# Kernel optimization log

Measured on AMD Instinct MI355X. Metric: run time of the kernel, lower is better.

Reference implementation:

```python
import jax, jax.numpy as jnp
import numpy as np

HID = 64
HEADS = 4
HEAD_DIM = HID // HEADS
N_MOL, N_PROT = 2048, 4096
E_MOL, E_PROT = 32768, 131072
B = 32


def _lin(key, din, dout):
    kw, kb = jax.random.split(key)
    s = 1.0 / np.sqrt(din)
    W = jax.random.uniform(kw, (din, dout), jnp.float32, -s, s)
    b = jax.random.uniform(kb, (dout,), jnp.float32, -s, s)
    return W, b


def setup_inputs() -> dict:
    key = jax.random.key(0)
    ks = jax.random.split(key, 32)
    inp = {}
    inp['mol_x'] = jax.random.normal(ks[0], (N_MOL, 11), jnp.float32)
    inp['prot_x'] = jax.random.normal(ks[1], (N_PROT, 15), jnp.float32)
    inp['mol_eattr'] = jax.random.normal(ks[2], (E_MOL, 10), jnp.float32)
    inp['prot_eattr'] = jax.random.normal(ks[3], (E_PROT, 10), jnp.float32)
    inp['mol_edge_index'] = jax.random.randint(ks[4], (2, E_MOL), 0, N_MOL, jnp.int32)
    inp['prot_edge_index'] = jax.random.randint(ks[5], (2, E_PROT), 0, N_PROT, jnp.int32)
    inp['mol_batch'] = jnp.sort(jax.random.randint(ks[6], (N_MOL,), 0, B, jnp.int32))
    inp['prot_batch'] = jnp.sort(jax.random.randint(ks[7], (N_PROT,), 0, B, jnp.int32))
    inp['node_lin_mol_W'], inp['node_lin_mol_b'] = _lin(ks[8], 11, HID)
    inp['node_lin_prot_W'], inp['node_lin_prot_b'] = _lin(ks[9], 15, HID)
    inp['edge_lin_mol_W'], inp['edge_lin_mol_b'] = _lin(ks[10], 10, HID)
    inp['edge_lin_prot_W'], inp['edge_lin_prot_b'] = _lin(ks[11], 10, HID)
    for pref, base in (('mol_conv', 12), ('prot_conv', 15)):
        W1s, b1s, W2s, b2s = [], [], [], []
        for l in range(3):
            k1, k2 = jax.random.split(ks[base + l])
            W1, b1 = _lin(k1, HID, HID)
            W2, b2 = _lin(k2, HID, HID)
            W1s.append(W1); b1s.append(b1); W2s.append(W2); b2s.append(b2)
        inp[pref + '_W1'] = jnp.stack(W1s); inp[pref + '_b1'] = jnp.stack(b1s)
        inp[pref + '_W2'] = jnp.stack(W2s); inp[pref + '_b2'] = jnp.stack(b2s)
    for pref, base in (('attn_mp', 18), ('attn_pm', 21)):
        Ws, bs = [], []
        for i in range(3):  # Q, K, V
            W, b = _lin(ks[base + i], HID, HID)
            Ws.append(W); bs.append(b)
        inp[pref + '_W'] = jnp.stack(Ws); inp[pref + '_b'] = jnp.stack(bs)
    inp['fc1_W'], inp['fc1_b'] = _lin(ks[24], 2 * HID, HID)
    inp['fc2_W'], inp['fc2_b'] = _lin(ks[25], HID, 1)
    return inp


def _gine_layer(x, src, dst, eattr, W1, b1, W2, b2):
    # message: ReLU(x_j + e_ji); GINEConv sum aggregation; eps = 0
    msg = jax.nn.relu(x[src] + eattr)                       # [E, H]
    agg = jax.ops.segment_sum(msg, dst, num_segments=x.shape[0])
    h = x + agg
    h = jax.nn.relu(h @ W1 + b1) @ W2 + b2                  # inner MLP
    return jax.nn.relu(h)                                   # post-conv ReLU


def _cross_attn(qn, kn, W, b):
    Nq, Nk = qn.shape[0], kn.shape[0]
    Q = (qn @ W[0] + b[0]).reshape(Nq, HEADS, HEAD_DIM)
    K = (kn @ W[1] + b[1]).reshape(Nk, HEADS, HEAD_DIM)
    V = (kn @ W[2] + b[2]).reshape(Nk, HEADS, HEAD_DIM)
    scores = jnp.einsum('qhd,khd->hqk', Q, K) / np.sqrt(HEAD_DIM)
    w = jax.nn.softmax(scores, axis=-1)
    out = jnp.einsum('hqk,khd->qhd', w, V)
    return out.reshape(Nq, HID)


def _pool(H, batch):
    s = jax.ops.segment_sum(H, batch, num_segments=B)
    c = jax.ops.segment_sum(jnp.ones((H.shape[0],), H.dtype), batch, num_segments=B)
    return s / jnp.maximum(c, 1.0)[:, None]


def _forward(mol_x, prot_x, mol_eattr, prot_eattr,
             node_lin_mol_W, node_lin_mol_b, node_lin_prot_W, node_lin_prot_b,
             edge_lin_mol_W, edge_lin_mol_b, edge_lin_prot_W, edge_lin_prot_b,
             mol_conv_W1, mol_conv_b1, mol_conv_W2, mol_conv_b2,
             prot_conv_W1, prot_conv_b1, prot_conv_W2, prot_conv_b2,
             attn_mp_W, attn_mp_b, attn_pm_W, attn_pm_b,
             fc1_W, fc1_b, fc2_W, fc2_b,
             mol_edge_index, prot_edge_index, mol_batch, prot_batch):
    xm = mol_x @ node_lin_mol_W + node_lin_mol_b
    xp = prot_x @ node_lin_prot_W + node_lin_prot_b
    em = mol_eattr @ edge_lin_mol_W + edge_lin_mol_b
    ep = prot_eattr @ edge_lin_prot_W + edge_lin_prot_b
    ms, md = mol_edge_index[0], mol_edge_index[1]
    ps, pd = prot_edge_index[0], prot_edge_index[1]
    for l in range(3):
        xm = _gine_layer(xm, ms, md, em, mol_conv_W1[l], mol_conv_b1[l], mol_conv_W2[l], mol_conv_b2[l])
    for l in range(3):
        xp = _gine_layer(xp, ps, pd, ep, prot_conv_W1[l], prot_conv_b1[l], prot_conv_W2[l], prot_conv_b2[l])
    H_mol = xm + _cross_attn(xm, xp, attn_mp_W, attn_mp_b)
    H_prot = xp + _cross_attn(xp, xm, attn_pm_W, attn_pm_b)
    z = jnp.concatenate([_pool(H_mol, mol_batch), _pool(H_prot, prot_batch)], axis=1)
    h = jax.nn.relu(z @ fc1_W + fc1_b)
    return jax.nn.sigmoid(h @ fc2_W + fc2_b).squeeze(-1)


def reference(mol_x, prot_x, mol_eattr, prot_eattr,
              node_lin_mol_W, node_lin_mol_b, node_lin_prot_W, node_lin_prot_b,
              edge_lin_mol_W, edge_lin_mol_b, edge_lin_prot_W, edge_lin_prot_b,
              mol_conv_W1, mol_conv_b1, mol_conv_W2, mol_conv_b2,
              prot_conv_W1, prot_conv_b1, prot_conv_W2, prot_conv_b2,
              attn_mp_W, attn_mp_b, attn_pm_W, attn_pm_b,
              fc1_W, fc1_b, fc2_W, fc2_b,
              mol_edge_index, prot_edge_index, mol_batch, prot_batch):
    return _forward(mol_x, prot_x, mol_eattr, prot_eattr,
                    node_lin_mol_W, node_lin_mol_b, node_lin_prot_W, node_lin_prot_b,
                    edge_lin_mol_W, edge_lin_mol_b, edge_lin_prot_W, edge_lin_prot_b,
                    mol_conv_W1, mol_conv_b1, mol_conv_W2, mol_conv_b2,
                    prot_conv_W1, prot_conv_b1, prot_conv_W2, prot_conv_b2,
                    attn_mp_W, attn_mp_b, attn_pm_W, attn_pm_b,
                    fc1_W, fc1_b, fc2_W, fc2_b,
                    mol_edge_index, prot_edge_index, mol_batch, prot_batch)
```

## Files before the change

### kernel.cpp

```cpp
#include <hip/hip_runtime.h>
#include <math.h>

#define HID 64
#define HEADS 4
#define HDIM 16
#define N_MOL 2048
#define N_PROT 4096
#define E_MOL 32768
#define E_PROT 131072
#define BATCH 32
#define N_TOT (N_MOL + N_PROT)
#define E_TOT (E_MOL + E_PROT)

#define TQA 16
#define TKA 32
#define KSTA 68
#define CH_MOL 4
#define CH_PROT 2
#define KCHUNK 1024
#define NGRP_MOL (N_MOL / TQA)

#define EPW 4

#define DOT4(a, b) ((a).x*(b).x + (a).y*(b).y + (a).z*(b).z + (a).w*(b).w)
#define EXP2(x) __builtin_amdgcn_exp2f(x)

__global__ void k_nl(const float* __restrict__ mol_x, const float* __restrict__ prot_x,
                     const float* __restrict__ Wm, const float* __restrict__ bm,
                     const float* __restrict__ Wp, const float* __restrict__ bp,
                     float* __restrict__ xm, float* __restrict__ xp) {
    int w = threadIdx.x >> 6, t = threadIdx.x & 63;
    int n = blockIdx.x * 4 + w;
    if (n < N_MOL) {
        const float* xr = mol_x + n * 11;
        float acc = bm[t];
#pragma unroll
        for (int i = 0; i < 11; ++i) acc += xr[i] * Wm[i * HID + t];
        xm[n * HID + t] = acc;
    } else {
        int p = n - N_MOL;
        const float* xr = prot_x + p * 15;
        float acc = bp[t];
#pragma unroll
        for (int i = 0; i < 15; ++i) acc += xr[i] * Wp[i * HID + t];
        xp[p * HID + t] = acc;
    }
}

__global__ __launch_bounds__(256) void k_msg(
    const float* __restrict__ xm, const float* __restrict__ xp,
    const float* __restrict__ mol_ea, const float* __restrict__ prot_ea,
    const int* __restrict__ mol_ei, const int* __restrict__ prot_ei,
    const float* __restrict__ Wem, const float* __restrict__ bem,
    const float* __restrict__ Wep, const float* __restrict__ bep,
    float* __restrict__ agg_m, float* __restrict__ agg_p) {
    int t = threadIdx.x & 63, w = threadIdx.x >> 6;
    int eb = blockIdx.x * (4 * EPW) + w * EPW;
    const float* x; const float* ea; const int* ei;
    const float* We; const float* be; float* agg; int E;
    if (eb < E_MOL) {
        x = xm; ea = mol_ea; ei = mol_ei; We = Wem; be = bem; agg = agg_m; E = E_MOL;
    } else {
        eb -= E_MOL;
        x = xp; ea = prot_ea; ei = prot_ei; We = Wep; be = bep; agg = agg_p; E = E_PROT;
    }
    float bt = be[t];
    float wcol[10];
#pragma unroll
    for (int i = 0; i < 10; ++i) wcol[i] = We[i * HID + t];

    int s[EPW], d[EPW];
    float2 a[EPW][5];
#pragma unroll
    for (int i = 0; i < EPW; ++i) {
        int e = eb + i;
        s[i] = ei[e];
        d[i] = ei[E + e];
        const float2* p = (const float2*)(ea + (size_t)e * 10);
#pragma unroll
        for (int j = 0; j < 5; ++j) a[i][j] = p[j];
    }
#pragma unroll
    for (int i = 0; i < EPW; ++i) {
        float m = bt;
#pragma unroll
        for (int j = 0; j < 5; ++j) {
            m = fmaf(a[i][j].x, wcol[2 * j], m);
            m = fmaf(a[i][j].y, wcol[2 * j + 1], m);
        }
        float msg = fmaxf(m + x[(size_t)s[i] * HID + t], 0.f);
        unsafeAtomicAdd(&agg[(size_t)d[i] * HID + t], msg);
    }
}

__global__ void k_node(const float* __restrict__ xin_m, const float* __restrict__ xin_p,
                       float* __restrict__ xout_m, float* __restrict__ xout_p,
                       float* __restrict__ agg_m, float* __restrict__ agg_p,
                       const float* __restrict__ W1m, const float* __restrict__ b1m,
                       const float* __restrict__ W2m, const float* __restrict__ b2m,
                       const float* __restrict__ W1p, const float* __restrict__ b1p,
                       const float* __restrict__ W2p, const float* __restrict__ b2p,
                       int doProj,
                       const float* __restrict__ mpW, const float* __restrict__ mpb,
                       const float* __restrict__ pmW, const float* __restrict__ pmb,
                       float* __restrict__ Qm, float* __restrict__ Kp, float* __restrict__ Vp,
                       float* __restrict__ Qp, float* __restrict__ Km, float* __restrict__ Vm) {
    __shared__ float h0[8][HID];
    __shared__ float h1[8][HID];
    int w = threadIdx.x >> 6, t = threadIdx.x & 63;
    int nb0 = blockIdx.x * 8 + w * 2;
    bool isMol = nb0 < N_MOL;
    const float* x  = isMol ? xin_m : xin_p;
    float* xo       = isMol ? xout_m : xout_p;
    float* agg      = isMol ? agg_m : agg_p;
    int nbias = isMol ? 0 : N_MOL;
    int n0 = nb0 - nbias;

#pragma unroll
    for (int u = 0; u < 2; ++u) {
        size_t idx = (size_t)(n0 + u) * HID + t;
        h0[w * 2 + u][t] = x[idx] + agg[idx];
        agg[idx] = 0.f;
    }

    const float* W1 = isMol ? W1m : W1p;
    const float* W2 = isMol ? W2m : W2p;
    float b1v = isMol ? b1m[t] : b1p[t];
    float b2v = isMol ? b2m[t] : b2p[t];
    float acc0 = b1v, acc1 = b1v;
    const float4* hA = (const float4*)h0[w * 2];
    const float4* hB = (const float4*)h0[w * 2 + 1];
#pragma unroll
    for (int k = 0; k < 16; ++k) {
        float4 a = hA[k], b = hB[k];
        float w0 = W1[(4 * k + 0) * HID + t], w1 = W1[(4 * k + 1) * HID + t];
        float w2 = W1[(4 * k + 2) * HID + t], w3 = W1[(4 * k + 3) * HID + t];
        acc0 = fmaf(a.x, w0, acc0); acc1 = fmaf(b.x, w0, acc1);
        acc0 = fmaf(a.y, w1, acc0); acc1 = fmaf(b.y, w1, acc1);
        acc0 = fmaf(a.z, w2, acc0); acc1 = fmaf(b.z, w2, acc1);
        acc0 = fmaf(a.w, w3, acc0); acc1 = fmaf(b.w, w3, acc1);
    }
    h1[w * 2][t] = fmaxf(acc0, 0.f);
    h1[w * 2 + 1][t] = fmaxf(acc1, 0.f);
    float d0 = b2v, d1 = b2v;
    const float4* gA = (const float4*)h1[w * 2];
    const float4* gB = (const float4*)h1[w * 2 + 1];
#pragma unroll
    for (int k = 0; k < 16; ++k) {
        float4 a = gA[k], b = gB[k];
        float w0 = W2[(4 * k + 0) * HID + t], w1 = W2[(4 * k + 1) * HID + t];
        float w2 = W2[(4 * k + 2) * HID + t], w3 = W2[(4 * k + 3) * HID + t];
        d0 = fmaf(a.x, w0, d0); d1 = fmaf(b.x, w0, d1);
        d0 = fmaf(a.y, w1, d0); d1 = fmaf(b.y, w1, d1);
        d0 = fmaf(a.z, w2, d0); d1 = fmaf(b.z, w2, d1);
        d0 = fmaf(a.w, w3, d0); d1 = fmaf(b.w, w3, d1);
    }
    float xv0 = fmaxf(d0, 0.f), xv1 = fmaxf(d1, 0.f);
    xo[n0 * HID + t] = xv0;
    xo[(n0 + 1) * HID + t] = xv1;

    if (doProj) {
        h0[w * 2][t] = xv0;
        h0[w * 2 + 1][t] = xv1;
        const float *WQ, *bQ, *WK, *bK, *WV, *bV;
        float *dQ, *dK, *dV;
        if (isMol) { WQ = mpW;        bQ = mpb;       WK = pmW + 4096; bK = pmb + 64;
                     WV = pmW + 8192; bV = pmb + 128; dQ = Qm; dK = Km; dV = Vm; }
        else       { WQ = pmW;        bQ = pmb;       WK = mpW + 4096; bK = mpb + 64;
                     WV = mpW + 8192; bV = mpb + 128; dQ = Qp; dK = Kp; dV = Vp; }
        float aQ0 = bQ[t], aQ1 = aQ0;
        float aK0 = bK[t], aK1 = aK0;
        float aV0 = bV[t], aV1 = aV0;
        const float4* rA = (const float4*)h0[w * 2];
        const float4* rB = (const float4*)h0[w * 2 + 1];
#pragma unroll
        for (int k = 0; k < 16; ++k) {
            float4 a = rA[k], b = rB[k];
#pragma unroll
            for (int j = 0; j < 4; ++j) {
                float av = (j == 0) ? a.x : (j == 1) ? a.y : (j == 2) ? a.z : a.w;
                float bv = (j == 0) ? b.x : (j == 1) ? b.y : (j == 2) ? b.z : b.w;
                float wq = WQ[(4 * k + j) * HID + t];
                float wk = WK[(4 * k + j) * HID + t];
                float wv = WV[(4 * k + j) * HID + t];
                aQ0 = fmaf(av, wq, aQ0); aQ1 = fmaf(bv, wq, aQ1);
                aK0 = fmaf(av, wk, aK0); aK1 = fmaf(bv, wk, aK1);
                aV0 = fmaf(av, wv, aV0); aV1 = fmaf(bv, wv, aV1);
            }
        }
        dQ[n0 * HID + t] = aQ0; dQ[(n0 + 1) * HID + t] = aQ1;
        dK[n0 * HID + t] = aK0; dK[(n0 + 1) * HID + t] = aK1;
        dV[n0 * HID + t] = aV0; dV[(n0 + 1) * HID + t] = aV1;
    }
}

__device__ inline void upd4(float4& A, const float4 v0, const float4 v1,
                            float p0, float p1, float al) {
    A.x = fmaf(p1, v1.x, fmaf(p0, v0.x, A.x * al));
    A.y = fmaf(p1, v1.y, fmaf(p0, v0.y, A.y * al));
    A.z = fmaf(p1, v1.z, fmaf(p0, v0.z, A.z * al));
    A.w = fmaf(p1, v1.w, fmaf(p0, v0.w, A.w * al));
}
__device__ inline void merge4(float4& A, const float4 B, float c1, float c2) {
    A.x = A.x * c1 + B.x * c2;
    A.y = A.y * c1 + B.y * c2;
    A.z = A.z * c1 + B.z * c2;
    A.w = A.w * c1 + B.w * c2;
}
__device__ inline float4 shfl4(const float4 a, int off) {
    float4 r;
    r.x = __shfl_xor(a.x, off, 64); r.y = __shfl_xor(a.y, off, 64);
    r.z = __shfl_xor(a.z, off, 64); r.w = __shfl_xor(a.w, off, 64);
    return r;
}

__global__ __launch_bounds__(256) void k_attn(
    const float* __restrict__ Qm, const float* __restrict__ Kp, const float* __restrict__ Vp,
    const float* __restrict__ Qp, const float* __restrict__ Km, const float* __restrict__ Vm,
    float* __restrict__ part_m, float* __restrict__ part_p) {
    __shared__ float Kl[2][TKA * KSTA];
    __shared__ float Vl[2][TKA * KSTA];

    int t = threadIdx.x;
    const float *Q, *K, *V;
    float* part;
    int q0, chunk, CH;
    {
        int b = blockIdx.x;
        const int MOLB = NGRP_MOL * CH_MOL;
        if (b < MOLB) {
            chunk = b & 3; q0 = (b >> 2) * TQA; CH = CH_MOL;
            Q = Qm; K = Kp; V = Vp; part = part_m;
        } else {
            b -= MOLB;
            chunk = b & 1; q0 = (b >> 1) * TQA; CH = CH_PROT;
            Q = Qp; K = Km; V = Vm; part = part_p;
        }
    }
    int kbeg = chunk * KCHUNK;

    int sub = t & 15, h = (t >> 4) & 3, qg = t >> 6;
    int r0 = t >> 4;
    int c0 = (t & 15) << 2;

    const float sc = 0.25f * 1.44269504088896f;
    float4 q4[4][4];
#pragma unroll
    for (int qq = 0; qq < 4; ++qq) {
        const float4* Qr = (const float4*)(Q + (q0 + qg * 4 + qq) * HID + h * HDIM);
#pragma unroll
        for (int j = 0; j < 4; ++j) {
            float4 v = Qr[j];
            v.x *= sc; v.y *= sc; v.z *= sc; v.w *= sc;
            q4[qq][j] = v;
        }
    }

    float mreg[4], lreg[4];
    float4 A[4][4];
#pragma unroll
    for (int qq = 0; qq < 4; ++qq) {
        mreg[qq] = -INFINITY; lreg[qq] = 0.f;
#pragma unroll
        for (int j = 0; j < 4; ++j) A[qq][j] = (float4){0.f, 0.f, 0.f, 0.f};
    }

    {
        const float4* Kg = (const float4*)(K + kbeg * HID);
        const float4* Vg = (const float4*)(V + kbeg * HID);
        float4 ka = Kg[t], kb = Kg[t + 256];
        float4 va = Vg[t], vb = Vg[t + 256];
        *(float4*)&Kl[0][r0 * KSTA + c0] = ka;
        *(float4*)&Kl[0][(r0 + 16) * KSTA + c0] = kb;
        *(float4*)&Vl[0][r0 * KSTA + c0] = va;
        *(float4*)&Vl[0][(r0 + 16) * KSTA + c0] = vb;
    }
    __syncthreads();

    const int NT = KCHUNK / TKA;
    for (int tile = 0; tile < NT; ++tile) {
        int cur = tile & 1;
        float4 ka, kb, va, vb;
        bool more = (tile + 1) < NT;
        if (more) {
            const float4* Kg = (const float4*)(K + (kbeg + (tile + 1) * TKA) * HID);
            const float4* Vg = (const float4*)(V + (kbeg + (tile + 1) * TKA) * HID);
            ka = Kg[t]; kb = Kg[t + 256];
            va = Vg[t]; vb = Vg[t + 256];
        }

        const float4* Kr0 = (const float4*)&Kl[cur][sub * KSTA + h * HDIM];
        const float4* Kr1 = (const float4*)&Kl[cur][(sub + 16) * KSTA + h * HDIM];
        float4 x0 = Kr0[0], x1 = Kr0[1], x2 = Kr0[2], x3 = Kr0[3];
        float4 y0 = Kr1[0], y1 = Kr1[1], y2 = Kr1[2], y3 = Kr1[3];

        float s0[4], s1[4];
#pragma unroll
        for (int qq = 0; qq < 4; ++qq) {
            s0[qq] = DOT4(x0, q4[qq][0]) + DOT4(x1, q4[qq][1]) + DOT4(x2, q4[qq][2]) + DOT4(x3, q4[qq][3]);
            s1[qq] = DOT4(y0, q4[qq][0]) + DOT4(y1, q4[qq][1]) + DOT4(y2, q4[qq][2]) + DOT4(y3, q4[qq][3]);
        }

        const float4* Vr0 = (const float4*)&Vl[cur][sub * KSTA + h * HDIM];
        const float4* Vr1 = (const float4*)&Vl[cur][(sub + 16) * KSTA + h * HDIM];
        float4 v00 = Vr0[0], v01 = Vr0[1], v02 = Vr0[2], v03 = Vr0[3];
        float4 v10 = Vr1[0], v11 = Vr1[1], v12 = Vr1[2], v13 = Vr1[3];

#pragma unroll
        for (int qq = 0; qq < 4; ++qq) {
            float mn = fmaxf(mreg[qq], fmaxf(s0[qq], s1[qq]));
            float al = EXP2(mreg[qq] - mn);
            float p0 = EXP2(s0[qq] - mn);
            float p1 = EXP2(s1[qq] - mn);
            lreg[qq] = lreg[qq] * al + p0 + p1;
            upd4(A[qq][0], v00, v10, p0, p1, al);
            upd4(A[qq][1], v01, v11, p0, p1, al);
            upd4(A[qq][2], v02, v12, p0, p1, al);
            upd4(A[qq][3], v03, v13, p0, p1, al);
            mreg[qq] = mn;
        }

        if (more) {
            int nxt = cur ^ 1;
            *(float4*)&Kl[nxt][r0 * KSTA + c0] = ka;
            *(float4*)&Kl[nxt][(r0 + 16) * KSTA + c0] = kb;
            *(float4*)&Vl[nxt][r0 * KSTA + c0] = va;
            *(float4*)&Vl[nxt][(r0 + 16) * KSTA + c0] = vb;
        }
        __syncthreads();
    }

#pragma unroll
    for (int off = 1; off < 16; off <<= 1) {
#pragma unroll
        for (int qq = 0; qq < 4; ++qq) {
            float m2 = __shfl_xor(mreg[qq], off, 64);
            float l2 = __shfl_xor(lreg[qq], off, 64);
            float4 B0 = shfl4(A[qq][0], off), B1 = shfl4(A[qq][1], off);
            float4 B2 = shfl4(A[qq][2], off), B3 = shfl4(A[qq][3], off);
            float mn = fmaxf(mreg[qq], m2);
            float c1 = EXP2(mreg[qq] - mn), c2 = EXP2(m2 - mn);
            lreg[qq] = lreg[qq] * c1 + l2 * c2;
            merge4(A[qq][0], B0, c1, c2); merge4(A[qq][1], B1, c1, c2);
            merge4(A[qq][2], B2, c1, c2); merge4(A[qq][3], B3, c1, c2);
            mreg[qq] = mn;
        }
    }

    if (sub == 0) {
#pragma unroll
        for (int qq = 0; qq < 4; ++qq) {
            int qi = q0 + qg * 4 + qq;
            float* pp = part + (size_t)((qi * HEADS + h) * CH + chunk) * 20;
            pp[0] = mreg[qq]; pp[1] = lreg[qq];
            *(float4*)&pp[4] = A[qq][0]; *(float4*)&pp[8] = A[qq][1];
            *(float4*)&pp[12] = A[qq][2]; *(float4*)&pp[16] = A[qq][3];
        }
    }
}

__global__ void k_pool(const float* __restrict__ part_m, const float* __restrict__ part_p,
                       const float* __restrict__ xm, const float* __restrict__ xp,
                       const int* __restrict__ mb, const int* __restrict__ pb,
                       float* __restrict__ pool, float* __restrict__ cnt) {
    __shared__ float sm[64][65];
    int b = blockIdx.x >> 3, sl = blockIdx.x & 7;
    int t = threadIdx.x;
    int h = t & 3, s = t >> 2;
    int ms, me, ps, pe;
    {
        int lo = 0, hi = N_MOL;
        while (lo < hi) { int mid = (lo + hi) >> 1; if (mb[mid] < b) lo = mid + 1; else hi = mid; }
        ms = lo; lo = ms; hi = N_MOL;
        while (lo < hi) { int mid = (lo + hi) >> 1; if (mb[mid] < b + 1) lo = mid + 1; else hi = mid; }
        me = lo;
        lo = 0; hi = N_PROT;
        while (lo < hi) { int mid = (lo + hi) >> 1; if (pb[mid] < b) lo = mid + 1; else hi = mid; }
        ps = lo; lo = ps; hi = N_PROT;
        while (lo < hi) { int mid = (lo + hi) >> 1; if (pb[mid] < b + 1) lo = mid + 1; else hi = mid; }
        pe = lo;
    }
    if (sl == 0 && t == 0) { cnt[b * 2] = (float)(me - ms); cnt[b * 2 + 1] = (float)(pe - ps); }

    {
        float acc[16];
#pragma unroll
        for (int d = 0; d < 16; ++d) acc[d] = 0.f;
        for (int q = ms + sl + 8 * s; q < me; q += 8 * 64) {
            const float* p0 = part_m + (size_t)(q * HEADS + h) * CH_MOL * 20;
            float mmax = -INFINITY;
#pragma unroll
            for (int c = 0; c < CH_MOL; ++c) mmax = fmaxf(mmax, p0[c * 20]);
            float lsum = 0.f, wgt[CH_MOL];
#pragma unroll
            for (int c = 0; c < CH_MOL; ++c) {
                wgt[c] = EXP2(p0[c * 20] - mmax);
                lsum += p0[c * 20 + 1] * wgt[c];
            }
            float inv = 1.f / lsum;
            const float* Xr = xm + q * HID + h * HDIM;
#pragma unroll
            for (int d = 0; d < 16; ++d) {
                float o = Xr[d];
#pragma unroll
                for (int c = 0; c < CH_MOL; ++c)
                    o = fmaf(p0[c * 20 + 4 + d], wgt[c] * inv, o);
                acc[d] += o;
            }
        }
#pragma unroll
        for (int d = 0; d < 16; ++d) sm[s][h * 16 + d] = acc[d];
    }
    __syncthreads();
    if (t < 64) {
        float sum = 0.f;
        for (int ss = 0; ss < 64; ++ss) sum += sm[ss][t];
        unsafeAtomicAdd(&pool[b * 128 + t], sum);
    }
    __syncthreads();

    {
        float acc[16];
#pragma unroll
        for (int d = 0; d < 16; ++d) acc[d] = 0.f;
        for (int q = ps + sl + 8 * s; q < pe; q += 8 * 64) {
            const float* p0 = part_p + (size_t)(q * HEADS + h) * CH_PROT * 20;
            float m0 = p0[0], m1 = p0[20];
            float mmax = fmaxf(m0, m1);
            float w0 = EXP2(m0 - mmax), w1 = EXP2(m1 - mmax);
            float inv = 1.f / (p0[1] * w0 + p0[21] * w1);
            w0 *= inv; w1 *= inv;
            const float* Xr = xp + q * HID + h * HDIM;
#pragma unroll
            for (int d = 0; d < 16; ++d)
                acc[d] += Xr[d] + p0[4 + d] * w0 + p0[24 + d] * w1;
        }
#pragma unroll
        for (int d = 0; d < 16; ++d) sm[s][h * 16 + d] = acc[d];
    }
    __syncthreads();
    if (t < 64) {
        float sum = 0.f;
        for (int ss = 0; ss < 64; ++ss) sum += sm[ss][t];
        unsafeAtomicAdd(&pool[b * 128 + 64 + t], sum);
    }
}

__global__ void k_head(const float* __restrict__ pool, const float* __restrict__ cnt,
                       const float* __restrict__ fc1W, const float* __restrict__ fc1b,
                       const float* __restrict__ fc2W, const float* __restrict__ fc2b,
                       float* __restrict__ out) {
    __shared__ float z[128];
    int b = blockIdx.x, t = threadIdx.x;
    float cm = fmaxf(cnt[b * 2 + 0], 1.f), cp = fmaxf(cnt[b * 2 + 1], 1.f);
    z[t] = pool[b * 128 + t] / cm;
    z[64 + t] = pool[b * 128 + 64 + t] / cp;
    __syncthreads();
    float acc = fc1b[t];
    const float4* zv = (const float4*)z;
#pragma unroll
    for (int k = 0; k < 32; ++k) {
        float4 hv = zv[k];
        acc = fmaf(hv.x, fc1W[(4 * k + 0) * 64 + t], acc);
        acc = fmaf(hv.y, fc1W[(4 * k + 1) * 64 + t], acc);
        acc = fmaf(hv.z, fc1W[(4 * k + 2) * 64 + t], acc);
        acc = fmaf(hv.w, fc1W[(4 * k + 3) * 64 + t], acc);
    }
    float hv = fmaxf(acc, 0.f);
    float prod = hv * fc2W[t];
#pragma unroll
    for (int off = 32; off > 0; off >>= 1) prod += __shfl_xor(prod, off, 64);
    if (t == 0) out[b] = 1.f / (1.f + __expf(-(prod + fc2b[0])));
}

extern "C" void kernel_launch(void* const* d_in, const int* in_sizes, int n_in,
                              void* d_out, int out_size, void* d_ws, size_t ws_size,
                              hipStream_t stream) {
    const float* mol_x   = (const float*)d_in[0];
    const float* prot_x  = (const float*)d_in[1];
    const float* mol_ea  = (const float*)d_in[2];
    const float* prot_ea = (const float*)d_in[3];
    const int*   mol_ei  = (const int*)d_in[4];
    const int*   prot_ei = (const int*)d_in[5];
    const int*   mol_b   = (const int*)d_in[6];
    const int*   prot_b  = (const int*)d_in[7];
    const float* nlmW = (const float*)d_in[8];
    const float* nlmb = (const float*)d_in[9];
    const float* nlpW = (const float*)d_in[10];
    const float* nlpb = (const float*)d_in[11];
    const float* elmW = (const float*)d_in[12];
    const float* elmb = (const float*)d_in[13];
    const float* elpW = (const float*)d_in[14];
    const float* elpb = (const float*)d_in[15];
    const float* mcW1 = (const float*)d_in[16];
    const float* mcb1 = (const float*)d_in[17];
    const float* mcW2 = (const float*)d_in[18];
    const float* mcb2 = (const float*)d_in[19];
    const float* pcW1 = (const float*)d_in[20];
    const float* pcb1 = (const float*)d_in[21];
    const float* pcW2 = (const float*)d_in[22];
    const float* pcb2 = (const float*)d_in[23];
    const float* mpW  = (const float*)d_in[24];
    const float* mpb  = (const float*)d_in[25];
    const float* pmW  = (const float*)d_in[26];
    const float* pmb  = (const float*)d_in[27];
    const float* fc1W = (const float*)d_in[28];
    const float* fc1b = (const float*)d_in[29];
    const float* fc2W = (const float*)d_in[30];
    const float* fc2b = (const float*)d_in[31];

    float* ws    = (float*)d_ws;
    float* xa_m  = ws;
    float* xa_p  = xa_m + 131072;
    float* xb_m  = xa_p + 262144;
    float* xb_p  = xb_m + 131072;
    float* Qm    = xb_p + 262144;
    float* Kp    = Qm + 131072;
    float* Vp    = Kp + 262144;
    float* Qp    = Vp + 262144;
    float* Km    = Qp + 262144;
    float* Vm    = Km + 131072;
    float* partm = Vm + 131072;
    float* partp = partm + 655360;
    float* pool  = partp + 655360;
    float* cnt   = pool + 4096;
    float* agg_m = partm;
    float* agg_p = partm + 131072;

    hipMemsetAsync(pool, 0, (size_t)(4096 + 64) * 4, stream);
    hipMemsetAsync(agg_m, 0, (size_t)(131072 + 262144) * 4, stream);

    k_nl<<<N_TOT / 4, 256, 0, stream>>>(mol_x, prot_x, nlmW, nlmb, nlpW, nlpb, xa_m, xa_p);

    k_msg<<<E_TOT / (4 * EPW), 256, 0, stream>>>(xa_m, xa_p, mol_ea, prot_ea, mol_ei, prot_ei,
        elmW, elmb, elpW, elpb, agg_m, agg_p);
    k_node<<<N_TOT / 8, 256, 0, stream>>>(xa_m, xa_p, xb_m, xb_p, agg_m, agg_p,
        mcW1, mcb1, mcW2, mcb2, pcW1, pcb1, pcW2, pcb2,
        0, mpW, mpb, pmW, pmb, Qm, Kp, Vp, Qp, Km, Vm);
    k_msg<<<E_TOT / (4 * EPW), 256, 0, stream>>>(xb_m, xb_p, mol_ea, prot_ea, mol_ei, prot_ei,
        elmW, elmb, elpW, elpb, agg_m, agg_p);
    k_node<<<N_TOT / 8, 256, 0, stream>>>(xb_m, xb_p, xa_m, xa_p, agg_m, agg_p,
        mcW1 + 4096, mcb1 + 64, mcW2 + 4096, mcb2 + 64,
        pcW1 + 4096, pcb1 + 64, pcW2 + 4096, pcb2 + 64,
        0, mpW, mpb, pmW, pmb, Qm, Kp, Vp, Qp, Km, Vm);
    k_msg<<<E_TOT / (4 * EPW), 256, 0, stream>>>(xa_m, xa_p, mol_ea, prot_ea, mol_ei, prot_ei,
        elmW, elmb, elpW, elpb, agg_m, agg_p);
    k_node<<<N_TOT / 8, 256, 0, stream>>>(xa_m, xa_p, xb_m, xb_p, agg_m, agg_p,
        mcW1 + 8192, mcb1 + 128, mcW2 + 8192, mcb2 + 128,
        pcW1 + 8192, pcb1 + 128, pcW2 + 8192, pcb2 + 128,
        1, mpW, mpb, pmW, pmb, Qm, Kp, Vp, Qp, Km, Vm);

    k_attn<<<NGRP_MOL * CH_MOL + (N_PROT / TQA) * CH_PROT, 256, 0, stream>>>(
        Qm, Kp, Vp, Qp, Km, Vm, partm, partp);

    k_pool<<<BATCH * 8, 256, 0, stream>>>(partm, partp, xb_m, xb_p, mol_b, prot_b, pool, cnt);
    k_head<<<BATCH, 64, 0, stream>>>(pool, cnt, fc1W, fc1b, fc2W, fc2b, (float*)d_out);
}
```

Before: 371.8 us.

## Fuse GNN front-end into cooperative kernel with CSR-style gather aggregation

Replaces the node-linear, three message-scatter and three node-update launches with one cooperative kernel that uses grid syncs between stages. Instead of scattering edge messages with float atomics, it builds per-destination edge lists with an atomic cursor (capped at CAP entries per node). Each node pair then gathers and sums its incoming messages in registers before the MLP. This removes launch overhead, the atomic float traffic and the aggregation-buffer memsets. In exchange it adds grid-wide barriers, can overflow the list if a node's in-degree exceeds CAP, and makes the summation order depend on edge arrival order. Load balance now follows per-node in-degree.

```diff
diff --git a/kernel.cpp b/kernel.cpp
--- a/kernel.cpp
+++ b/kernel.cpp
@@ -1,5 +1,8 @@
 #include <hip/hip_runtime.h>
+#include <hip/hip_cooperative_groups.h>
 #include <math.h>
+
+namespace cg = cooperative_groups;
 
 #define HID 64
 #define HEADS 4
@@ -11,6 +14,7 @@
 #define BATCH 32
 #define N_TOT (N_MOL + N_PROT)
 #define E_TOT (E_MOL + E_PROT)
+#define CAP 128
 
 #define TQA 16
 #define TKA 32
@@ -20,10 +24,505 @@
 #define KCHUNK 1024
 #define NGRP_MOL (N_MOL / TQA)
 
+#define FRONT_BLKS 1024
+#define FRONT_WAVES (FRONT_BLKS * 4)
+
 #define EPW 4
 
 #define DOT4(a, b) ((a).x*(b).x + (a).y*(b).y + (a).z*(b).z + (a).w*(b).w)
 #define EXP2(x) __builtin_amdgcn_exp2f(x)
+
+struct Params {
+    const float *mol_x, *prot_x, *mol_ea, *prot_ea;
+    const int   *mol_ei, *prot_ei, *mol_b, *prot_b;
+    const float *nlmW, *nlmb, *nlpW, *nlpb;
+    const float *elmW, *elmb, *elpW, *elpb;
+    const float *mcW1, *mcb1, *mcW2, *mcb2;
+    const float *pcW1, *pcb1, *pcW2, *pcb2;
+    const float *mpW, *mpb, *pmW, *pmb;
+    float *xa_m, *xa_p, *xb_m, *xb_p;
+    float *Qm, *Kp, *Vp, *Qp, *Km, *Vm;
+    int *cursor, *eidx;
+};
+
+__device__ inline void upd4(float4& A, const float4 v0, const float4 v1,
+                            float p0, float p1, float al) {
+    A.x = fmaf(p1, v1.x, fmaf(p0, v0.x, A.x * al));
+    A.y = fmaf(p1, v1.y, fmaf(p0, v0.y, A.y * al));
+    A.z = fmaf(p1, v1.z, fmaf(p0, v0.z, A.z * al));
+    A.w = fmaf(p1, v1.w, fmaf(p0, v0.w, A.w * al));
+}
+__device__ inline void merge4(float4& A, const float4 B, float c1, float c2) {
+    A.x = A.x * c1 + B.x * c2;
+    A.y = A.y * c1 + B.y * c2;
+    A.z = A.z * c1 + B.z * c2;
+    A.w = A.w * c1 + B.w * c2;
+}
+__device__ inline float4 shfl4(const float4 a, int off) {
+    float4 r;
+    r.x = __shfl_xor(a.x, off, 64); r.y = __shfl_xor(a.y, off, 64);
+    r.z = __shfl_xor(a.z, off, 64); r.w = __shfl_xor(a.w, off, 64);
+    return r;
+}
+
+__device__ __forceinline__ void gine_pair(
+    float* smem, int pr, int w, int t,
+    const float* xin_m, const float* xin_p,
+    float* xout_m, float* xout_p,
+    const float* mol_ea, const float* prot_ea,
+    const int* mol_ei, const int* prot_ei,
+    const float* Wem, const float* bem, const float* Wep, const float* bep,
+    const float* W1m, const float* b1m, const float* W2m, const float* b2m,
+    const float* W1p, const float* b1p, const float* W2p, const float* b2p,
+    const int* cnt, const int* eidx,
+    int doProj,
+    const float* mpW, const float* mpb, const float* pmW, const float* pmb,
+    float* Qm, float* Kp, float* Vp, float* Qp, float* Km, float* Vm) {
+    int nb0 = pr * 2;
+    bool isMol = nb0 < N_MOL;
+    const float* x  = isMol ? xin_m : xin_p;
+    float* xo       = isMol ? xout_m : xout_p;
+    const float* We = isMol ? Wem : Wep;
+    float bt        = isMol ? bem[t] : bep[t];
+    const float* ea_base = isMol ? mol_ea : prot_ea;
+    const int* srcarr    = isMol ? mol_ei : prot_ei;
+    int nbias = isMol ? 0 : N_MOL;
+    int n0 = nb0 - nbias;
+    float* h0 = smem + (size_t)(w * 2) * HID;
+    float* h1 = smem + 512 + (size_t)(w * 2) * HID;
+    float wcol[10];
+#pragma unroll
+    for (int i = 0; i < 10; ++i) wcol[i] = We[i * HID + t];
+
+#pragma unroll
+    for (int u = 0; u < 2; ++u) {
+        int nb = nb0 + u;
+        int deg = cnt[nb];
+        const int* lst = eidx + (size_t)nb * CAP;
+        float agg = 0.f;
+        int j = 0;
+        for (; j + 1 < deg; j += 2) {
+            int e0 = lst[j], e1 = lst[j + 1];
+            int s0 = srcarr[e0], s1 = srcarr[e1];
+            const float2* p0 = (const float2*)(ea_base + (size_t)e0 * 10);
+            const float2* p1 = (const float2*)(ea_base + (size_t)e1 * 10);
+            float2 a0 = p0[0], a1 = p0[1], a2 = p0[2], a3 = p0[3], a4 = p0[4];
+            float2 c0 = p1[0], c1 = p1[1], c2 = p1[2], c3 = p1[3], c4 = p1[4];
+            float xs0 = x[s0 * HID + t];
+            float xs1 = x[s1 * HID + t];
+            float m0 = bt, m1 = bt;
+            m0 = fmaf(a0.x, wcol[0], m0); m0 = fmaf(a0.y, wcol[1], m0);
+            m0 = fmaf(a1.x, wcol[2], m0); m0 = fmaf(a1.y, wcol[3], m0);
+            m0 = fmaf(a2.x, wcol[4], m0); m0 = fmaf(a2.y, wcol[5], m0);
+            m0 = fmaf(a3.x, wcol[6], m0); m0 = fmaf(a3.y, wcol[7], m0);
+            m0 = fmaf(a4.x, wcol[8], m0); m0 = fmaf(a4.y, wcol[9], m0);
+            m1 = fmaf(c0.x, wcol[0], m1); m1 = fmaf(c0.y, wcol[1], m1);
+            m1 = fmaf(c1.x, wcol[2], m1); m1 = fmaf(c1.y, wcol[3], m1);
+            m1 = fmaf(c2.x, wcol[4], m1); m1 = fmaf(c2.y, wcol[5], m1);
+            m1 = fmaf(c3.x, wcol[6], m1); m1 = fmaf(c3.y, wcol[7], m1);
+            m1 = fmaf(c4.x, wcol[8], m1); m1 = fmaf(c4.y, wcol[9], m1);
+            agg += fmaxf(m0 + xs0, 0.f) + fmaxf(m1 + xs1, 0.f);
+        }
+        if (j < deg) {
+            int e0 = lst[j];
+            int s0 = srcarr[e0];
+            const float2* p0 = (const float2*)(ea_base + (size_t)e0 * 10);
+            float2 a0 = p0[0], a1 = p0[1], a2 = p0[2], a3 = p0[3], a4 = p0[4];
+            float xs0 = x[s0 * HID + t];
+            float m0 = bt;
+            m0 = fmaf(a0.x, wcol[0], m0); m0 = fmaf(a0.y, wcol[1], m0);
+            m0 = fmaf(a1.x, wcol[2], m0); m0 = fmaf(a1.y, wcol[3], m0);
+            m0 = fmaf(a2.x, wcol[4], m0); m0 = fmaf(a2.y, wcol[5], m0);
+            m0 = fmaf(a3.x, wcol[6], m0); m0 = fmaf(a3.y, wcol[7], m0);
+            m0 = fmaf(a4.x, wcol[8], m0); m0 = fmaf(a4.y, wcol[9], m0);
+            agg += fmaxf(m0 + xs0, 0.f);
+        }
+        h0[u * HID + t] = x[(size_t)(n0 + u) * HID + t] + agg;
+    }
+
+    const float* W1 = isMol ? W1m : W1p;
+    const float* W2 = isMol ? W2m : W2p;
+    float b1v = isMol ? b1m[t] : b1p[t];
+    float b2v = isMol ? b2m[t] : b2p[t];
+    float acc0 = b1v, acc1 = b1v;
+    const float4* hA = (const float4*)h0;
+    const float4* hB = (const float4*)(h0 + HID);
+#pragma unroll
+    for (int k = 0; k < 16; ++k) {
+        float4 a = hA[k], b = hB[k];
+        float w0 = W1[(4 * k + 0) * HID + t], w1 = W1[(4 * k + 1) * HID + t];
+        float w2 = W1[(4 * k + 2) * HID + t], w3 = W1[(4 * k + 3) * HID + t];
+        acc0 = fmaf(a.x, w0, acc0); acc1 = fmaf(b.x, w0, acc1);
+        acc0 = fmaf(a.y, w1, acc0); acc1 = fmaf(b.y, w1, acc1);
+        acc0 = fmaf(a.z, w2, acc0); acc1 = fmaf(b.z, w2, acc1);
+        acc0 = fmaf(a.w, w3, acc0); acc1 = fmaf(b.w, w3, acc1);
+    }
+    h1[t] = fmaxf(acc0, 0.f);
+    h1[HID + t] = fmaxf(acc1, 0.f);
+    float d0 = b2v, d1 = b2v;
+    const float4* gA = (const float4*)h1;
+    const float4* gB = (const float4*)(h1 + HID);
+#pragma unroll
+    for (int k = 0; k < 16; ++k) {
+        float4 a = gA[k], b = gB[k];
+        float w0 = W2[(4 * k + 0) * HID + t], w1 = W2[(4 * k + 1) * HID + t];
+        float w2 = W2[(4 * k + 2) * HID + t], w3 = W2[(4 * k + 3) * HID + t];
+        d0 = fmaf(a.x, w0, d0); d1 = fmaf(b.x, w0, d1);
+        d0 = fmaf(a.y, w1, d0); d1 = fmaf(b.y, w1, d1);
+        d0 = fmaf(a.z, w2, d0); d1 = fmaf(b.z, w2, d1);
+        d0 = fmaf(a.w, w3, d0); d1 = fmaf(b.w, w3, d1);
+    }
+    float xv0 = fmaxf(d0, 0.f), xv1 = fmaxf(d1, 0.f);
+    xo[(size_t)n0 * HID + t] = xv0;
+    xo[(size_t)(n0 + 1) * HID + t] = xv1;
+
+    if (doProj) {
+        h0[t] = xv0;
+        h0[HID + t] = xv1;
+        const float *WQ, *bQ, *WK, *bK, *WV, *bV;
+        float *dQ, *dK, *dV;
+        if (isMol) { WQ = mpW;        bQ = mpb;       WK = pmW + 4096; bK = pmb + 64;
+                     WV = pmW + 8192; bV = pmb + 128; dQ = Qm; dK = Km; dV = Vm; }
+        else       { WQ = pmW;        bQ = pmb;       WK = mpW + 4096; bK = mpb + 64;
+                     WV = mpW + 8192; bV = mpb + 128; dQ = Qp; dK = Kp; dV = Vp; }
+        float aQ0 = bQ[t], aQ1 = aQ0;
+        float aK0 = bK[t], aK1 = aK0;
+        float aV0 = bV[t], aV1 = aV0;
+        const float4* rA = (const float4*)h0;
+        const float4* rB = (const float4*)(h0 + HID);
+#pragma unroll
+        for (int k = 0; k < 16; ++k) {
+            float4 a = rA[k], b = rB[k];
+#pragma unroll
+            for (int j = 0; j < 4; ++j) {
+                float av = (j == 0) ? a.x : (j == 1) ? a.y : (j == 2) ? a.z : a.w;
+                float bv = (j == 0) ? b.x : (j == 1) ? b.y : (j == 2) ? b.z : b.w;
+                float wq = WQ[(4 * k + j) * HID + t];
+                float wk = WK[(4 * k + j) * HID + t];
+                float wv = WV[(4 * k + j) * HID + t];
+                aQ0 = fmaf(av, wq, aQ0); aQ1 = fmaf(bv, wq, aQ1);
+                aK0 = fmaf(av, wk, aK0); aK1 = fmaf(bv, wk, aK1);
+                aV0 = fmaf(av, wv, aV0); aV1 = fmaf(bv, wv, aV1);
+            }
+        }
+        dQ[(size_t)n0 * HID + t] = aQ0; dQ[(size_t)(n0 + 1) * HID + t] = aQ1;
+        dK[(size_t)n0 * HID + t] = aK0; dK[(size_t)(n0 + 1) * HID + t] = aK1;
+        dV[(size_t)n0 * HID + t] = aV0; dV[(size_t)(n0 + 1) * HID + t] = aV1;
+    }
+}
+
+__global__ __launch_bounds__(256, 4) void k_front(Params p) {
+    cg::grid_group grid = cg::this_grid();
+    __shared__ __align__(16) float smem[1024];
+    int tid = threadIdx.x;
+    int t = tid & 63, w = tid >> 6;
+    int bid = blockIdx.x;
+    int gw = bid * 4 + w;
+
+    {
+        int idx = bid * 256 + tid;
+        if (idx < N_TOT + 4096 + 64) p.cursor[idx] = 0;
+    }
+    for (int n = gw; n < N_TOT; n += FRONT_WAVES) {
+        if (n < N_MOL) {
+            const float* xr = p.mol_x + n * 11;
+            float acc = p.nlmb[t];
+#pragma unroll
+            for (int i = 0; i < 11; ++i) acc += xr[i] * p.nlmW[i * HID + t];
+            p.xa_m[(size_t)n * HID + t] = acc;
+        } else {
+            int q = n - N_MOL;
+            const float* xr = p.prot_x + q * 15;
+            float acc = p.nlpb[t];
+#pragma unroll
+            for (int i = 0; i < 15; ++i) acc += xr[i] * p.nlpW[i * HID + t];
+            p.xa_p[(size_t)q * HID + t] = acc;
+        }
+    }
+    grid.sync();
+
+    {
+        int e = bid * 256 + tid;
+        if (e < E_TOT) {
+            int node, loc;
+            if (e < E_MOL) { node = p.mol_ei[E_MOL + e]; loc = e; }
+            else { int el = e - E_MOL; node = N_MOL + p.prot_ei[E_PROT + el]; loc = el; }
+            int pos = atomicAdd(&p.cursor[node], 1);
+            p.eidx[(size_t)node * CAP + pos] = loc;
+        }
+    }
+    grid.sync();
+
+    if (gw < N_TOT / 2)
+        gine_pair(smem, gw, w, t, p.xa_m, p.xa_p, p.xb_m, p.xb_p,
+                  p.mol_ea, p.prot_ea, p.mol_ei, p.prot_ei,
+                  p.elmW, p.elmb, p.elpW, p.elpb,
+                  p.mcW1, p.mcb1, p.mcW2, p.mcb2, p.pcW1, p.pcb1, p.pcW2, p.pcb2,
+                  p.cursor, p.eidx, 0, p.mpW, p.mpb, p.pmW, p.pmb,
+                  p.Qm, p.Kp, p.Vp, p.Qp, p.Km, p.Vm);
+    grid.sync();
+    if (gw < N_TOT / 2)
+        gine_pair(smem, gw, w, t, p.xb_m, p.xb_p, p.xa_m, p.xa_p,
+                  p.mol_ea, p.prot_ea, p.mol_ei, p.prot_ei,
+                  p.elmW, p.elmb, p.elpW, p.elpb,
+                  p.mcW1 + 4096, p.mcb1 + 64, p.mcW2 + 4096, p.mcb2 + 64,
+                  p.pcW1 + 4096, p.pcb1 + 64, p.pcW2 + 4096, p.pcb2 + 64,
+                  p.cursor, p.eidx, 0, p.mpW, p.mpb, p.pmW, p.pmb,
+                  p.Qm, p.Kp, p.Vp, p.Qp, p.Km, p.Vm);
+    grid.sync();
+    if (gw < N_TOT / 2)
+        gine_pair(smem, gw, w, t, p.xa_m, p.xa_p, p.xb_m, p.xb_p,
+                  p.mol_ea, p.prot_ea, p.mol_ei, p.prot_ei,
+                  p.elmW, p.elmb, p.elpW, p.elpb,
+                  p.mcW1 + 8192, p.mcb1 + 128, p.mcW2 + 8192, p.mcb2 + 128,
+                  p.pcW1 + 8192, p.pcb1 + 128, p.pcW2 + 8192, p.pcb2 + 128,
+                  p.cursor, p.eidx, 1, p.mpW, p.mpb, p.pmW, p.pmb,
+                  p.Qm, p.Kp, p.Vp, p.Qp, p.Km, p.Vm);
+}
+
+__global__ __launch_bounds__(256) void k_attn(
+    const float* __restrict__ Qm, const float* __restrict__ Kp, const float* __restrict__ Vp,
+    const float* __restrict__ Qp, const float* __restrict__ Km, const float* __restrict__ Vm,
+    float* __restrict__ part_m, float* __restrict__ part_p) {
+    __shared__ float Kl[2][TKA * KSTA];
+    __shared__ float Vl[2][TKA * KSTA];
+    int t = threadIdx.x;
+    const float *Q, *K, *V;
+    float* part;
+    int q0, chunk, CH;
+    {
+        int b = blockIdx.x;
+        const int MOLB = NGRP_MOL * CH_MOL;
+        if (b < MOLB) {
+            chunk = b & 3; q0 = (b >> 2) * TQA; CH = CH_MOL;
+            Q = Qm; K = Kp; V = Vp; part = part_m;
+        } else {
+            b -= MOLB;
+            chunk = b & 1; q0 = (b >> 1) * TQA; CH = CH_PROT;
+            Q = Qp; K = Km; V = Vm; part = part_p;
+        }
+    }
+    int kbeg = chunk * KCHUNK;
+    int sub = t & 15, h = (t >> 4) & 3, qg = t >> 6;
+    int r0 = t >> 4;
+    int c0 = (t & 15) << 2;
+    const float sc = 0.25f * 1.44269504088896f;
+    float4 q4[4][4];
+#pragma unroll
+    for (int qq = 0; qq < 4; ++qq) {
+        const float4* Qr = (const float4*)(Q + (q0 + qg * 4 + qq) * HID + h * HDIM);
+#pragma unroll
+        for (int j = 0; j < 4; ++j) {
+            float4 v = Qr[j];
+            v.x *= sc; v.y *= sc; v.z *= sc; v.w *= sc;
+            q4[qq][j] = v;
+        }
+    }
+    float mreg[4], lreg[4];
+    float4 A[4][4];
+#pragma unroll
+    for (int qq = 0; qq < 4; ++qq) {
+        mreg[qq] = -INFINITY; lreg[qq] = 0.f;
+#pragma unroll
+        for (int j = 0; j < 4; ++j) A[qq][j] = (float4){0.f, 0.f, 0.f, 0.f};
+    }
+    {
+        const float4* Kg = (const float4*)(K + kbeg * HID);
+        const float4* Vg = (const float4*)(V + kbeg * HID);
+        float4 ka = Kg[t], kb = Kg[t + 256];
+        float4 va = Vg[t], vb = Vg[t + 256];
+        *(float4*)&Kl[0][r0 * KSTA + c0] = ka;
+        *(float4*)&Kl[0][(r0 + 16) * KSTA + c0] = kb;
+        *(float4*)&Vl[0][r0 * KSTA + c0] = va;
+        *(float4*)&Vl[0][(r0 + 16) * KSTA + c0] = vb;
+    }
+    __syncthreads();
+    const int NT = KCHUNK / TKA;
+    for (int tile = 0; tile < NT; ++tile) {
+        int cur = tile & 1;
+        float4 ka, kb, va, vb;
+        bool more = (tile + 1) < NT;
+        if (more) {
+            const float4* Kg = (const float4*)(K + (kbeg + (tile + 1) * TKA) * HID);
+            const float4* Vg = (const float4*)(V + (kbeg + (tile + 1) * TKA) * HID);
+            ka = Kg[t]; kb = Kg[t + 256];
+            va = Vg[t]; vb = Vg[t + 256];
+        }
+        const float4* Kr0 = (const float4*)&Kl[cur][sub * KSTA + h * HDIM];
+        const float4* Kr1 = (const float4*)&Kl[cur][(sub + 16) * KSTA + h * HDIM];
+        float4 x0 = Kr0[0], x1 = Kr0[1], x2 = Kr0[2], x3 = Kr0[3];
+        float4 y0 = Kr1[0], y1 = Kr1[1], y2 = Kr1[2], y3 = Kr1[3];
+        float s0[4], s1[4];
+#pragma unroll
+        for (int qq = 0; qq < 4; ++qq) {
+            s0[qq] = DOT4(x0, q4[qq][0]) + DOT4(x1, q4[qq][1]) + DOT4(x2, q4[qq][2]) + DOT4(x3, q4[qq][3]);
+            s1[qq] = DOT4(y0, q4[qq][0]) + DOT4(y1, q4[qq][1]) + DOT4(y2, q4[qq][2]) + DOT4(y3, q4[qq][3]);
+        }
+        const float4* Vr0 = (const float4*)&Vl[cur][sub * KSTA + h * HDIM];
+        const float4* Vr1 = (const float4*)&Vl[cur][(sub + 16) * KSTA + h * HDIM];
+        float4 v00 = Vr0[0], v01 = Vr0[1], v02 = Vr0[2], v03 = Vr0[3];
+        float4 v10 = Vr1[0], v11 = Vr1[1], v12 = Vr1[2], v13 = Vr1[3];
+#pragma unroll
+        for (int qq = 0; qq < 4; ++qq) {
+            float mn = fmaxf(mreg[qq], fmaxf(s0[qq], s1[qq]));
+            float al = EXP2(mreg[qq] - mn);
+            float p0 = EXP2(s0[qq] - mn);
+            float p1 = EXP2(s1[qq] - mn);
+            lreg[qq] = lreg[qq] * al + p0 + p1;
+            upd4(A[qq][0], v00, v10, p0, p1, al);
+            upd4(A[qq][1], v01, v11, p0, p1, al);
+            upd4(A[qq][2], v02, v12, p0, p1, al);
+            upd4(A[qq][3], v03, v13, p0, p1, al);
+            mreg[qq] = mn;
+        }
+        if (more) {
+            int nxt = cur ^ 1;
+            *(float4*)&Kl[nxt][r0 * KSTA + c0] = ka;
+            *(float4*)&Kl[nxt][(r0 + 16) * KSTA + c0] = kb;
+            *(float4*)&Vl[nxt][r0 * KSTA + c0] = va;
+            *(float4*)&Vl[nxt][(r0 + 16) * KSTA + c0] = vb;
+        }
+        __syncthreads();
+    }
+#pragma unroll
+    for (int off = 1; off < 16; off <<= 1) {
+#pragma unroll
+        for (int qq = 0; qq < 4; ++qq) {
+            float m2 = __shfl_xor(mreg[qq], off, 64);
+            float l2 = __shfl_xor(lreg[qq], off, 64);
+            float4 B0 = shfl4(A[qq][0], off), B1 = shfl4(A[qq][1], off);
+            float4 B2 = shfl4(A[qq][2], off), B3 = shfl4(A[qq][3], off);
+            float mn = fmaxf(mreg[qq], m2);
+            float c1 = EXP2(mreg[qq] - mn), c2 = EXP2(m2 - mn);
+            lreg[qq] = lreg[qq] * c1 + l2 * c2;
+            merge4(A[qq][0], B0, c1, c2); merge4(A[qq][1], B1, c1, c2);
+            merge4(A[qq][2], B2, c1, c2); merge4(A[qq][3], B3, c1, c2);
+            mreg[qq] = mn;
+        }
+    }
+    if (sub == 0) {
+#pragma unroll
+        for (int qq = 0; qq < 4; ++qq) {
+            int qi = q0 + qg * 4 + qq;
+            float* pp = part + (size_t)((qi * HEADS + h) * CH + chunk) * 20;
+            pp[0] = mreg[qq]; pp[1] = lreg[qq];
+            *(float4*)&pp[4] = A[qq][0]; *(float4*)&pp[8] = A[qq][1];
+            *(float4*)&pp[12] = A[qq][2]; *(float4*)&pp[16] = A[qq][3];
+        }
+    }
+}
+
+__global__ void k_pool(const float* __restrict__ part_m, const float* __restrict__ part_p,
+                       const float* __restrict__ xm, const float* __restrict__ xp,
+                       const int* __restrict__ mb, const int* __restrict__ pb,
+                       float* __restrict__ pool, float* __restrict__ cnt) {
+    __shared__ float sm[64][65];
+    int b = blockIdx.x >> 3, sl = blockIdx.x & 7;
+    int t = threadIdx.x;
+    int h = t & 3, s = t >> 2;
+    int ms, me, ps, pe;
+    {
+        int lo = 0, hi = N_MOL;
+        while (lo < hi) { int mid = (lo + hi) >> 1; if (mb[mid] < b) lo = mid + 1; else hi = mid; }
+        ms = lo; lo = ms; hi = N_MOL;
+        while (lo < hi) { int mid = (lo + hi) >> 1; if (mb[mid] < b + 1) lo = mid + 1; else hi = mid; }
+        me = lo;
+        lo = 0; hi = N_PROT;
+        while (lo < hi) { int mid = (lo + hi) >> 1; if (pb[mid] < b) lo = mid + 1; else hi = mid; }
+        ps = lo; lo = ps; hi = N_PROT;
+        while (lo < hi) { int mid = (lo + hi) >> 1; if (pb[mid] < b + 1) lo = mid + 1; else hi = mid; }
+        pe = lo;
+    }
+    if (sl == 0 && t == 0) { cnt[b * 2] = (float)(me - ms); cnt[b * 2 + 1] = (float)(pe - ps); }
+    {
+        float acc[16];
+#pragma unroll
+        for (int d = 0; d < 16; ++d) acc[d] = 0.f;
+        for (int q = ms + sl + 8 * s; q < me; q += 8 * 64) {
+            const float* p0 = part_m + (size_t)(q * HEADS + h) * CH_MOL * 20;
+            float mmax = -INFINITY;
+#pragma unroll
+            for (int c = 0; c < CH_MOL; ++c) mmax = fmaxf(mmax, p0[c * 20]);
+            float lsum = 0.f, wgt[CH_MOL];
+#pragma unroll
+            for (int c = 0; c < CH_MOL; ++c) {
+                wgt[c] = EXP2(p0[c * 20] - mmax);
+                lsum += p0[c * 20 + 1] * wgt[c];
+            }
+            float inv = 1.f / lsum;
+            const float* Xr = xm + q * HID + h * HDIM;
+#pragma unroll
+            for (int d = 0; d < 16; ++d) {
+                float o = Xr[d];
+#pragma unroll
+                for (int c = 0; c < CH_MOL; ++c)
+                    o = fmaf(p0[c * 20 + 4 + d], wgt[c] * inv, o);
+                acc[d] += o;
+            }
+        }
+#pragma unroll
+        for (int d = 0; d < 16; ++d) sm[s][h * 16 + d] = acc[d];
+    }
+    __syncthreads();
+    if (t < 64) {
+        float sum = 0.f;
+        for (int ss = 0; ss < 64; ++ss) sum += sm[ss][t];
+        unsafeAtomicAdd(&pool[b * 128 + t], sum);
+    }
+    __syncthreads();
+    {
+        float acc[16];
+#pragma unroll
+        for (int d = 0; d < 16; ++d) acc[d] = 0.f;
+        for (int q = ps + sl + 8 * s; q < pe; q += 8 * 64) {
+            const float* p0 = part_p + (size_t)(q * HEADS + h) * CH_PROT * 20;
+            float m0 = p0[0], m1 = p0[20];
+            float mmax = fmaxf(m0, m1);
+            float w0 = EXP2(m0 - mmax), w1 = EXP2(m1 - mmax);
+            float inv = 1.f / (p0[1] * w0 + p0[21] * w1);
+            w0 *= inv; w1 *= inv;
+            const float* Xr = xp + q * HID + h * HDIM;
+#pragma unroll
+            for (int d = 0; d < 16; ++d)
+                acc[d] += Xr[d] + p0[4 + d] * w0 + p0[24 + d] * w1;
+        }
+#pragma unroll
+        for (int d = 0; d < 16; ++d) sm[s][h * 16 + d] = acc[d];
+    }
+    __syncthreads();
+    if (t < 64) {
+        float sum = 0.f;
+        for (int ss = 0; ss < 64; ++ss) sum += sm[ss][t];
+        unsafeAtomicAdd(&pool[b * 128 + 64 + t], sum);
+    }
+}
+
+__global__ void k_head(const float* __restrict__ pool, const float* __restrict__ cnt,
+                       const float* __restrict__ fc1W, const float* __restrict__ fc1b,
+                       const float* __restrict__ fc2W, const float* __restrict__ fc2b,
+                       float* __restrict__ out) {
+    __shared__ float z[128];
+    int b = blockIdx.x, t = threadIdx.x;
+    float cm = fmaxf(cnt[b * 2 + 0], 1.f), cp = fmaxf(cnt[b * 2 + 1], 1.f);
+    z[t] = pool[b * 128 + t] / cm;
+    z[64 + t] = pool[b * 128 + 64 + t] / cp;
+    __syncthreads();
+    float acc = fc1b[t];
+    const float4* zv = (const float4*)z;
+#pragma unroll
+    for (int k = 0; k < 32; ++k) {
+        float4 hv = zv[k];
+        acc = fmaf(hv.x, fc1W[(4 * k + 0) * 64 + t], acc);
+        acc = fmaf(hv.y, fc1W[(4 * k + 1) * 64 + t], acc);
+        acc = fmaf(hv.z, fc1W[(4 * k + 2) * 64 + t], acc);
+        acc = fmaf(hv.w, fc1W[(4 * k + 3) * 64 + t], acc);
+    }
+    float hv = fmaxf(acc, 0.f);
+    float prod = hv * fc2W[t];
+#pragma unroll
+    for (int off = 32; off > 0; off >>= 1) prod += __shfl_xor(prod, off, 64);
+    if (t == 0) out[b] = 1.f / (1.f + __expf(-(prod + fc2b[0])));
+}
 
 __global__ void k_nl(const float* __restrict__ mol_x, const float* __restrict__ prot_x,
                      const float* __restrict__ Wm, const float* __restrict__ bm,
@@ -38,12 +537,12 @@
         for (int i = 0; i < 11; ++i) acc += xr[i] * Wm[i * HID + t];
         xm[n * HID + t] = acc;
     } else {
-        int p = n - N_MOL;
-        const float* xr = prot_x + p * 15;
+        int q = n - N_MOL;
+        const float* xr = prot_x + q * 15;
         float acc = bp[t];
 #pragma unroll
         for (int i = 0; i < 15; ++i) acc += xr[i] * Wp[i * HID + t];
-        xp[p * HID + t] = acc;
+        xp[q * HID + t] = acc;
     }
 }
 
@@ -68,7 +567,6 @@
     float wcol[10];
 #pragma unroll
     for (int i = 0; i < 10; ++i) wcol[i] = We[i * HID + t];
-
     int s[EPW], d[EPW];
     float2 a[EPW][5];
 #pragma unroll
@@ -76,9 +574,9 @@
         int e = eb + i;
         s[i] = ei[e];
         d[i] = ei[E + e];
-        const float2* p = (const float2*)(ea + (size_t)e * 10);
-#pragma unroll
-        for (int j = 0; j < 5; ++j) a[i][j] = p[j];
+        const float2* pp = (const float2*)(ea + (size_t)e * 10);
+#pragma unroll
+        for (int j = 0; j < 5; ++j) a[i][j] = pp[j];
     }
 #pragma unroll
     for (int i = 0; i < EPW; ++i) {
@@ -115,14 +613,12 @@
     float* agg      = isMol ? agg_m : agg_p;
     int nbias = isMol ? 0 : N_MOL;
     int n0 = nb0 - nbias;
-
 #pragma unroll
     for (int u = 0; u < 2; ++u) {
         size_t idx = (size_t)(n0 + u) * HID + t;
         h0[w * 2 + u][t] = x[idx] + agg[idx];
         agg[idx] = 0.f;
     }
-
     const float* W1 = isMol ? W1m : W1p;
     const float* W2 = isMol ? W2m : W2p;
     float b1v = isMol ? b1m[t] : b1p[t];
@@ -158,7 +654,6 @@
     float xv0 = fmaxf(d0, 0.f), xv1 = fmaxf(d1, 0.f);
     xo[n0 * HID + t] = xv0;
     xo[(n0 + 1) * HID + t] = xv1;
-
     if (doProj) {
         h0[w * 2][t] = xv0;
         h0[w * 2 + 1][t] = xv1;
@@ -192,285 +687,6 @@
         dK[n0 * HID + t] = aK0; dK[(n0 + 1) * HID + t] = aK1;
         dV[n0 * HID + t] = aV0; dV[(n0 + 1) * HID + t] = aV1;
     }
-}
-
-__device__ inline void upd4(float4& A, const float4 v0, const float4 v1,
-                            float p0, float p1, float al) {
-    A.x = fmaf(p1, v1.x, fmaf(p0, v0.x, A.x * al));
-    A.y = fmaf(p1, v1.y, fmaf(p0, v0.y, A.y * al));
-    A.z = fmaf(p1, v1.z, fmaf(p0, v0.z, A.z * al));
-    A.w = fmaf(p1, v1.w, fmaf(p0, v0.w, A.w * al));
-}
-__device__ inline void merge4(float4& A, const float4 B, float c1, float c2) {
-    A.x = A.x * c1 + B.x * c2;
-    A.y = A.y * c1 + B.y * c2;
-    A.z = A.z * c1 + B.z * c2;
-    A.w = A.w * c1 + B.w * c2;
-}
-__device__ inline float4 shfl4(const float4 a, int off) {
-    float4 r;
-    r.x = __shfl_xor(a.x, off, 64); r.y = __shfl_xor(a.y, off, 64);
-    r.z = __shfl_xor(a.z, off, 64); r.w = __shfl_xor(a.w, off, 64);
-    return r;
-}
-
-__global__ __launch_bounds__(256) void k_attn(
-    const float* __restrict__ Qm, const float* __restrict__ Kp, const float* __restrict__ Vp,
-    const float* __restrict__ Qp, const float* __restrict__ Km, const float* __restrict__ Vm,
-    float* __restrict__ part_m, float* __restrict__ part_p) {
-    __shared__ float Kl[2][TKA * KSTA];
-    __shared__ float Vl[2][TKA * KSTA];
-
-    int t = threadIdx.x;
-    const float *Q, *K, *V;
-    float* part;
-    int q0, chunk, CH;
-    {
-        int b = blockIdx.x;
-        const int MOLB = NGRP_MOL * CH_MOL;
-        if (b < MOLB) {
-            chunk = b & 3; q0 = (b >> 2) * TQA; CH = CH_MOL;
-            Q = Qm; K = Kp; V = Vp; part = part_m;
-        } else {
-            b -= MOLB;
-            chunk = b & 1; q0 = (b >> 1) * TQA; CH = CH_PROT;
-            Q = Qp; K = Km; V = Vm; part = part_p;
-        }
-    }
-    int kbeg = chunk * KCHUNK;
-
-    int sub = t & 15, h = (t >> 4) & 3, qg = t >> 6;
-    int r0 = t >> 4;
-    int c0 = (t & 15) << 2;
-
-    const float sc = 0.25f * 1.44269504088896f;
-    float4 q4[4][4];
-#pragma unroll
-    for (int qq = 0; qq < 4; ++qq) {
-        const float4* Qr = (const float4*)(Q + (q0 + qg * 4 + qq) * HID + h * HDIM);
-#pragma unroll
-        for (int j = 0; j < 4; ++j) {
-            float4 v = Qr[j];
-            v.x *= sc; v.y *= sc; v.z *= sc; v.w *= sc;
-            q4[qq][j] = v;
-        }
-    }
-
-    float mreg[4], lreg[4];
-    float4 A[4][4];
-#pragma unroll
-    for (int qq = 0; qq < 4; ++qq) {
-        mreg[qq] = -INFINITY; lreg[qq] = 0.f;
-#pragma unroll
-        for (int j = 0; j < 4; ++j) A[qq][j] = (float4){0.f, 0.f, 0.f, 0.f};
-    }
-
-    {
-        const float4* Kg = (const float4*)(K + kbeg * HID);
-        const float4* Vg = (const float4*)(V + kbeg * HID);
-        float4 ka = Kg[t], kb = Kg[t + 256];
-        float4 va = Vg[t], vb = Vg[t + 256];
-        *(float4*)&Kl[0][r0 * KSTA + c0] = ka;
-        *(float4*)&Kl[0][(r0 + 16) * KSTA + c0] = kb;
-        *(float4*)&Vl[0][r0 * KSTA + c0] = va;
-        *(float4*)&Vl[0][(r0 + 16) * KSTA + c0] = vb;
-    }
-    __syncthreads();
-
-    const int NT = KCHUNK / TKA;
-    for (int tile = 0; tile < NT; ++tile) {
-        int cur = tile & 1;
-        float4 ka, kb, va, vb;
-        bool more = (tile + 1) < NT;
-        if (more) {
-            const float4* Kg = (const float4*)(K + (kbeg + (tile + 1) * TKA) * HID);
-            const float4* Vg = (const float4*)(V + (kbeg + (tile + 1) * TKA) * HID);
-            ka = Kg[t]; kb = Kg[t + 256];
-            va = Vg[t]; vb = Vg[t + 256];
-        }
-
-        const float4* Kr0 = (const float4*)&Kl[cur][sub * KSTA + h * HDIM];
-        const float4* Kr1 = (const float4*)&Kl[cur][(sub + 16) * KSTA + h * HDIM];
-        float4 x0 = Kr0[0], x1 = Kr0[1], x2 = Kr0[2], x3 = Kr0[3];
-        float4 y0 = Kr1[0], y1 = Kr1[1], y2 = Kr1[2], y3 = Kr1[3];
-
-        float s0[4], s1[4];
-#pragma unroll
-        for (int qq = 0; qq < 4; ++qq) {
-            s0[qq] = DOT4(x0, q4[qq][0]) + DOT4(x1, q4[qq][1]) + DOT4(x2, q4[qq][2]) + DOT4(x3, q4[qq][3]);
-            s1[qq] = DOT4(y0, q4[qq][0]) + DOT4(y1, q4[qq][1]) + DOT4(y2, q4[qq][2]) + DOT4(y3, q4[qq][3]);
-        }
-
-        const float4* Vr0 = (const float4*)&Vl[cur][sub * KSTA + h * HDIM];
-        const float4* Vr1 = (const float4*)&Vl[cur][(sub + 16) * KSTA + h * HDIM];
-        float4 v00 = Vr0[0], v01 = Vr0[1], v02 = Vr0[2], v03 = Vr0[3];
-        float4 v10 = Vr1[0], v11 = Vr1[1], v12 = Vr1[2], v13 = Vr1[3];
-
-#pragma unroll
-        for (int qq = 0; qq < 4; ++qq) {
-            float mn = fmaxf(mreg[qq], fmaxf(s0[qq], s1[qq]));
-            float al = EXP2(mreg[qq] - mn);
-            float p0 = EXP2(s0[qq] - mn);
-            float p1 = EXP2(s1[qq] - mn);
-            lreg[qq] = lreg[qq] * al + p0 + p1;
-            upd4(A[qq][0], v00, v10, p0, p1, al);
-            upd4(A[qq][1], v01, v11, p0, p1, al);
-            upd4(A[qq][2], v02, v12, p0, p1, al);
-            upd4(A[qq][3], v03, v13, p0, p1, al);
-            mreg[qq] = mn;
-        }
-
-        if (more) {
-            int nxt = cur ^ 1;
-            *(float4*)&Kl[nxt][r0 * KSTA + c0] = ka;
-            *(float4*)&Kl[nxt][(r0 + 16) * KSTA + c0] = kb;
-            *(float4*)&Vl[nxt][r0 * KSTA + c0] = va;
-            *(float4*)&Vl[nxt][(r0 + 16) * KSTA + c0] = vb;
-        }
-        __syncthreads();
-    }
-
-#pragma unroll
-    for (int off = 1; off < 16; off <<= 1) {
-#pragma unroll
-        for (int qq = 0; qq < 4; ++qq) {
-            float m2 = __shfl_xor(mreg[qq], off, 64);
-            float l2 = __shfl_xor(lreg[qq], off, 64);
-            float4 B0 = shfl4(A[qq][0], off), B1 = shfl4(A[qq][1], off);
-            float4 B2 = shfl4(A[qq][2], off), B3 = shfl4(A[qq][3], off);
-            float mn = fmaxf(mreg[qq], m2);
-            float c1 = EXP2(mreg[qq] - mn), c2 = EXP2(m2 - mn);
-            lreg[qq] = lreg[qq] * c1 + l2 * c2;
-            merge4(A[qq][0], B0, c1, c2); merge4(A[qq][1], B1, c1, c2);
-            merge4(A[qq][2], B2, c1, c2); merge4(A[qq][3], B3, c1, c2);
-            mreg[qq] = mn;
-        }
-    }
-
-    if (sub == 0) {
-#pragma unroll
-        for (int qq = 0; qq < 4; ++qq) {
-            int qi = q0 + qg * 4 + qq;
-            float* pp = part + (size_t)((qi * HEADS + h) * CH + chunk) * 20;
-            pp[0] = mreg[qq]; pp[1] = lreg[qq];
-            *(float4*)&pp[4] = A[qq][0]; *(float4*)&pp[8] = A[qq][1];
-            *(float4*)&pp[12] = A[qq][2]; *(float4*)&pp[16] = A[qq][3];
-        }
-    }
-}
-
-__global__ void k_pool(const float* __restrict__ part_m, const float* __restrict__ part_p,
-                       const float* __restrict__ xm, const float* __restrict__ xp,
-                       const int* __restrict__ mb, const int* __restrict__ pb,
-                       float* __restrict__ pool, float* __restrict__ cnt) {
-    __shared__ float sm[64][65];
-    int b = blockIdx.x >> 3, sl = blockIdx.x & 7;
-    int t = threadIdx.x;
-    int h = t & 3, s = t >> 2;
-    int ms, me, ps, pe;
-    {
-        int lo = 0, hi = N_MOL;
-        while (lo < hi) { int mid = (lo + hi) >> 1; if (mb[mid] < b) lo = mid + 1; else hi = mid; }
-        ms = lo; lo = ms; hi = N_MOL;
-        while (lo < hi) { int mid = (lo + hi) >> 1; if (mb[mid] < b + 1) lo = mid + 1; else hi = mid; }
-        me = lo;
-        lo = 0; hi = N_PROT;
-        while (lo < hi) { int mid = (lo + hi) >> 1; if (pb[mid] < b) lo = mid + 1; else hi = mid; }
-        ps = lo; lo = ps; hi = N_PROT;
-        while (lo < hi) { int mid = (lo + hi) >> 1; if (pb[mid] < b + 1) lo = mid + 1; else hi = mid; }
-        pe = lo;
-    }
-    if (sl == 0 && t == 0) { cnt[b * 2] = (float)(me - ms); cnt[b * 2 + 1] = (float)(pe - ps); }
-
-    {
-        float acc[16];
-#pragma unroll
-        for (int d = 0; d < 16; ++d) acc[d] = 0.f;
-        for (int q = ms + sl + 8 * s; q < me; q += 8 * 64) {
-            const float* p0 = part_m + (size_t)(q * HEADS + h) * CH_MOL * 20;
-            float mmax = -INFINITY;
-#pragma unroll
-            for (int c = 0; c < CH_MOL; ++c) mmax = fmaxf(mmax, p0[c * 20]);
-            float lsum = 0.f, wgt[CH_MOL];
-#pragma unroll
-            for (int c = 0; c < CH_MOL; ++c) {
-                wgt[c] = EXP2(p0[c * 20] - mmax);
-                lsum += p0[c * 20 + 1] * wgt[c];
-            }
-            float inv = 1.f / lsum;
-            const float* Xr = xm + q * HID + h * HDIM;
-#pragma unroll
-            for (int d = 0; d < 16; ++d) {
-                float o = Xr[d];
-#pragma unroll
-                for (int c = 0; c < CH_MOL; ++c)
-                    o = fmaf(p0[c * 20 + 4 + d], wgt[c] * inv, o);
-                acc[d] += o;
-            }
-        }
-#pragma unroll
-        for (int d = 0; d < 16; ++d) sm[s][h * 16 + d] = acc[d];
-    }
-    __syncthreads();
-    if (t < 64) {
-        float sum = 0.f;
-        for (int ss = 0; ss < 64; ++ss) sum += sm[ss][t];
-        unsafeAtomicAdd(&pool[b * 128 + t], sum);
-    }
-    __syncthreads();
-
-    {
-        float acc[16];
-#pragma unroll
-        for (int d = 0; d < 16; ++d) acc[d] = 0.f;
-        for (int q = ps + sl + 8 * s; q < pe; q += 8 * 64) {
-            const float* p0 = part_p + (size_t)(q * HEADS + h) * CH_PROT * 20;
-            float m0 = p0[0], m1 = p0[20];
-            float mmax = fmaxf(m0, m1);
-            float w0 = EXP2(m0 - mmax), w1 = EXP2(m1 - mmax);
-            float inv = 1.f / (p0[1] * w0 + p0[21] * w1);
-            w0 *= inv; w1 *= inv;
-            const float* Xr = xp + q * HID + h * HDIM;
-#pragma unroll
-            for (int d = 0; d < 16; ++d)
-                acc[d] += Xr[d] + p0[4 + d] * w0 + p0[24 + d] * w1;
-        }
-#pragma unroll
-        for (int d = 0; d < 16; ++d) sm[s][h * 16 + d] = acc[d];
-    }
-    __syncthreads();
-    if (t < 64) {
-        float sum = 0.f;
-        for (int ss = 0; ss < 64; ++ss) sum += sm[ss][t];
-        unsafeAtomicAdd(&pool[b * 128 + 64 + t], sum);
-    }
-}
-
-__global__ void k_head(const float* __restrict__ pool, const float* __restrict__ cnt,
-                       const float* __restrict__ fc1W, const float* __restrict__ fc1b,
-                       const float* __restrict__ fc2W, const float* __restrict__ fc2b,
-                       float* __restrict__ out) {
-    __shared__ float z[128];
-    int b = blockIdx.x, t = threadIdx.x;
-    float cm = fmaxf(cnt[b * 2 + 0], 1.f), cp = fmaxf(cnt[b * 2 + 1], 1.f);
-    z[t] = pool[b * 128 + t] / cm;
-    z[64 + t] = pool[b * 128 + 64 + t] / cp;
-    __syncthreads();
-    float acc = fc1b[t];
-    const float4* zv = (const float4*)z;
-#pragma unroll
-    for (int k = 0; k < 32; ++k) {
-        float4 hv = zv[k];
-        acc = fmaf(hv.x, fc1W[(4 * k + 0) * 64 + t], acc);
-        acc = fmaf(hv.y, fc1W[(4 * k + 1) * 64 + t], acc);
-        acc = fmaf(hv.z, fc1W[(4 * k + 2) * 64 + t], acc);
-        acc = fmaf(hv.w, fc1W[(4 * k + 3) * 64 + t], acc);
-    }
-    float hv = fmaxf(acc, 0.f);
-    float prod = hv * fc2W[t];
-#pragma unroll
-    for (int off = 32; off > 0; off >>= 1) prod += __shfl_xor(prod, off, 64);
-    if (t == 0) out[b] = 1.f / (1.f + __expf(-(prod + fc2b[0])));
 }
 
 extern "C" void kernel_launch(void* const* d_in, const int* in_sizes, int n_in,
@@ -522,16 +738,40 @@
     float* Vm    = Km + 131072;
     float* partm = Vm + 131072;
     float* partp = partm + 655360;
-    float* pool  = partp + 655360;
+    int* cursor  = (int*)(partp + 655360);
+    float* pool  = (float*)(cursor + N_TOT);
     float* cnt   = pool + 4096;
+    int* eidx    = (int*)partm;
     float* agg_m = partm;
     float* agg_p = partm + 131072;
 
-    hipMemsetAsync(pool, 0, (size_t)(4096 + 64) * 4, stream);
+    Params P;
+    P.mol_x = mol_x; P.prot_x = prot_x; P.mol_ea = mol_ea; P.prot_ea = prot_ea;
+    P.mol_ei = mol_ei; P.prot_ei = prot_ei; P.mol_b = mol_b; P.prot_b = prot_b;
+    P.nlmW = nlmW; P.nlmb = nlmb; P.nlpW = nlpW; P.nlpb = nlpb;
+    P.elmW = elmW; P.elmb = elmb; P.elpW = elpW; P.elpb = elpb;
+    P.mcW1 = mcW1; P.mcb1 = mcb1; P.mcW2 = mcW2; P.mcb2 = mcb2;
+    P.pcW1 = pcW1; P.pcb1 = pcb1; P.pcW2 = pcW2; P.pcb2 = pcb2;
+    P.mpW = mpW; P.mpb = mpb; P.pmW = pmW; P.pmb = pmb;
+    P.xa_m = xa_m; P.xa_p = xa_p; P.xb_m = xb_m; P.xb_p = xb_p;
+    P.Qm = Qm; P.Kp = Kp; P.Vp = Vp; P.Qp = Qp; P.Km = Km; P.Vm = Vm;
+    P.cursor = cursor; P.eidx = eidx;
+
+    void* args[] = { &P };
+    hipError_t err = hipLaunchCooperativeKernel((const void*)k_front,
+                                                dim3(FRONT_BLKS), dim3(256),
+                                                args, 0, stream);
+    if (err == hipSuccess) {
+        k_attn<<<NGRP_MOL * CH_MOL + (N_PROT / TQA) * CH_PROT, 256, 0, stream>>>(
+            Qm, Kp, Vp, Qp, Km, Vm, partm, partp);
+        k_pool<<<BATCH * 8, 256, 0, stream>>>(partm, partp, xb_m, xb_p, mol_b, prot_b, pool, cnt);
+        k_head<<<BATCH, 64, 0, stream>>>(pool, cnt, fc1W, fc1b, fc2W, fc2b, (float*)d_out);
+        return;
+    }
+
+    hipMemsetAsync(cursor, 0, (size_t)(N_TOT + 4096 + 64) * 4, stream);
     hipMemsetAsync(agg_m, 0, (size_t)(131072 + 262144) * 4, stream);
-
     k_nl<<<N_TOT / 4, 256, 0, stream>>>(mol_x, prot_x, nlmW, nlmb, nlpW, nlpb, xa_m, xa_p);
-
     k_msg<<<E_TOT / (4 * EPW), 256, 0, stream>>>(xa_m, xa_p, mol_ea, prot_ea, mol_ei, prot_ei,
         elmW, elmb, elpW, elpb, agg_m, agg_p);
     k_node<<<N_TOT / 8, 256, 0, stream>>>(xa_m, xa_p, xb_m, xb_p, agg_m, agg_p,
@@ -549,10 +789,8 @@
         mcW1 + 8192, mcb1 + 128, mcW2 + 8192, mcb2 + 128,
         pcW1 + 8192, pcb1 + 128, pcW2 + 8192, pcb2 + 128,
         1, mpW, mpb, pmW, pmb, Qm, Kp, Vp, Qp, Km, Vm);
-
     k_attn<<<NGRP_MOL * CH_MOL + (N_PROT / TQA) * CH_PROT, 256, 0, stream>>>(
         Qm, Kp, Vp, Qp, Km, Vm, partm, partp);
-
     k_pool<<<BATCH * 8, 256, 0, stream>>>(partm, partp, xb_m, xb_p, mol_b, prot_b, pool, cnt);
     k_head<<<BATCH, 64, 0, stream>>>(pool, cnt, fc1W, fc1b, fc2W, fc2b, (float*)d_out);
 }
```

Result: slower. 890.7 us (+139.6%).
